# Kernel optimization log

Hardware: AMD Instinct MI355X
Metric: run time of the kernel (lower is better)

The kernel has to match this reference:

```python
import jax, jax.numpy as jnp
import numpy as np
import math

D_K = 8  # = n_wires; one input value encoded per wire


def setup_inputs() -> dict:
    key = jax.random.key(0)
    k1, k2, k3, k4 = jax.random.split(key, 4)
    B, S, E = 4, 2048, 1024
    x = jax.random.normal(k1, (B, S, E), dtype=jnp.float32)
    theta = jax.random.normal(k2, (D_K,), dtype=jnp.float32)  # shared RX params (one ModuleList reused per head)
    W = jax.random.normal(k3, (E, E), dtype=jnp.float32) * (1.0 / math.sqrt(E))
    b = jax.random.normal(k4, (E,), dtype=jnp.float32) * 0.01
    return {"x": x, "theta": theta, "W": W, "b": b}


def reference(x, theta, W, b):
    B, S, E = x.shape
    dk = theta.shape[0]
    H = E // dk
    # Quantum circuit collapse: RX(x_i) then RX(theta_i) on |0>, measure PauliZ
    # on each wire of a product state -> <Z_i> = cos(x_i + theta_i).
    proj = x.reshape(B, S, H, dk)
    q_out = jnp.cos(proj + theta)  # theta broadcast over (B,S,H)
    # NOTE: faithful to original — attention is over the HEAD axis: (B,S,H,H)
    attn = jnp.einsum('bshd,bsgd->bshg', q_out, q_out) / math.sqrt(dk)
    attn = jax.nn.softmax(attn, axis=-1)  # dropout is identity at inference
    out = jnp.einsum('bshg,bsgd->bshd', attn, q_out)  # (B,S,H,dk)
    # faithful transpose(1,2).contiguous().view(B,S,E) reinterleave
    out = jnp.transpose(out, (0, 2, 1, 3)).reshape(B, S, E)
    return out @ W.T + b
```

## Files before the change

kernel.cpp:

```cpp
#include <hip/hip_runtime.h>
#include <hip/hip_bf16.h>
#include <stdint.h>

typedef __attribute__((ext_vector_type(8))) short bf16x8;
typedef __attribute__((ext_vector_type(4))) float f32x4;
typedef __attribute__((ext_vector_type(16))) float f32x16;
typedef __attribute__((ext_vector_type(2))) unsigned int uint32x2;
typedef __attribute__((address_space(3))) void lds_t;
typedef __attribute__((address_space(1))) void glb_t;

#define B_ 4
#define S_ 2048
#define E_ 1024
#define M_ (B_*S_)
#define QTS 152
#define PPB 2

static __device__ __forceinline__ ushort f2bf(float f) {
  uint32_t u = __float_as_uint(f);
  u += 0x7fffu + ((u >> 16) & 1u);
  return (ushort)(u >> 16);
}

static __device__ __forceinline__ uint32_t pk_bf16(float lo, float hi) {
  uint32_t r;
  asm("v_cvt_pk_bf16_f32 %0, %1, %2" : "=v"(r) : "v"(lo), "v"(hi));
  return r;
}
static __device__ __forceinline__ float fexp2(float x) {
  float r;
  asm("v_exp_f32 %0, %1" : "=v"(r) : "v"(x));
  return r;
}

static __device__ __forceinline__ void half_zip(uint32_t a, uint32_t b, bool convA,
                                                uint32_t& X, uint32_t& Y) {
  if (convA) {
    uint32x2 r = __builtin_amdgcn_permlane32_swap(b, a, false, false);
    Y = r[0]; X = r[1];
  } else {
    uint32x2 r = __builtin_amdgcn_permlane32_swap(a, b, false, false);
    X = r[0]; Y = r[1];
  }
}

__global__ __launch_bounds__(256) void qattn(const float* __restrict__ x,
                                             const float* __restrict__ theta,
                                             ushort* __restrict__ outr) {
  const int wave = threadIdx.x >> 6;
  const int lane = threadIdx.x & 63;
  const int l31 = lane & 31, hw = lane >> 5;

  const int bid = blockIdx.x;
  const int pair = (bid & 7) * 512 + (bid >> 3);

  __shared__ __align__(16) ushort qL[PPB][129 * 8];
  __shared__ __align__(16) ushort qT[PPB][16 * QTS];

  uint32x2 pr = __builtin_amdgcn_permlane32_swap((uint32_t)lane, (uint32_t)(lane + 1000),
                                                 false, false);
  const bool convA = (__builtin_amdgcn_readfirstlane((int)pr[0]) >= 1000);

  auto gen = [&](int bs_g, int sel) {
    ushort* qpg = qL[sel];
    ushort* qtg = qT[sel];
    const int h  = 32 * wave + (lane >> 1);
    const int dh = (lane & 1) * 4;
    const float4 xv = *(const float4*)(x + (size_t)bs_g * E_ + h * 8 + dh);
    float q[4];
    q[0] = __cosf(xv.x + theta[dh + 0]);
    q[1] = __cosf(xv.y + theta[dh + 1]);
    q[2] = __cosf(xv.z + theta[dh + 2]);
    q[3] = __cosf(xv.w + theta[dh + 3]);

    const float QS = 0.71419165f;
    uint2 pw;
    pw.x = pk_bf16(q[0] * QS, q[1] * QS);
    pw.y = pk_bf16(q[2] * QS, q[3] * QS);
    *(uint2*)(qpg + h * 8 + dh) = pw;

    #pragma unroll
    for (int j = 0; j < 4; ++j)
      qtg[(dh + j) * QTS + h] = f2bf(q[j]);
    #pragma unroll
    for (int j = 0; j < 4; ++j)
      qtg[(8 + dh + j) * QTS + h] = (j == 0) ? (ushort)0x3F80u : (ushort)0u;

    if (lane == 0) *(uint4*)(qpg + 128 * 8) = make_uint4(0, 0, 0, 0);
  };

  gen(pair * PPB + 0, 0);
  gen(pair * PPB + 1, 1);
  __syncthreads();
  __builtin_amdgcn_sched_barrier(0);

  const int hi = wave;
  const bf16x8 zf = {};

  #pragma unroll
  for (int pp = 0; pp < PPB; ++pp) {
    const ushort* qp = qL[pp];
    const ushort* qt = qT[pp];
    const int bs = pair * PPB + pp;
    const int b = bs >> 11, s = bs & 2047;

    bf16x8 aqv[4];
    #pragma unroll
    for (int gj = 0; gj < 4; ++gj) {
      const int arow = (lane < 32) ? (gj * 32 + l31) : 128;
      aqv[gj] = *(const bf16x8*)(qp + arow * 8);
    }
    const int brow = (lane < 32) ? (hi * 32 + l31) : 128;
    const bf16x8 bq = *(const bf16x8*)(qp + brow * 8);

    f32x16 oacc = {};

    #pragma unroll
    for (int gj = 0; gj < 4; ++gj) {
      f32x16 sc = {};
      sc = __builtin_amdgcn_mfma_f32_32x32x16_bf16(aqv[gj], bq, sc, 0, 0, 0);
      bf16x8 fA = *(const bf16x8*)(qt + (l31 & 15) * QTS + (gj * 2 + 0) * 16 + hw * 8);
      bf16x8 fB = *(const bf16x8*)(qt + (l31 & 15) * QTS + (gj * 2 + 1) * 16 + hw * 8);
      fA = (l31 < 16) ? fA : zf;
      fB = (l31 < 16) ? fB : zf;
      float pv[16];
      #pragma unroll
      for (int k = 0; k < 16; ++k) pv[k] = fexp2(sc[k]);
      #pragma unroll
      for (int sl = 0; sl < 2; ++sl) {
        const int pb = sl * 8;
        const uint32_t u = pk_bf16(pv[pb+0], pv[pb+1]);
        const uint32_t v = pk_bf16(pv[pb+2], pv[pb+3]);
        const uint32_t w = pk_bf16(pv[pb+4], pv[pb+5]);
        const uint32_t z = pk_bf16(pv[pb+6], pv[pb+7]);
        uint32_t f0, f1, f2, f3;
        half_zip(u, w, convA, f0, f2);
        half_zip(v, z, convA, f1, f3);
        uint32_t fr[4] = {f0, f1, f2, f3};
        oacc = __builtin_amdgcn_mfma_f32_32x32x16_bf16((sl == 0) ? fA : fB,
                                                       *(const bf16x8*)fr,
                                                       oacc, 0, 0, 0);
      }
    }

    const int scol = s & 127, srow = s >> 7;
    const float inv = __builtin_amdgcn_rcpf(oacc[4]);
    const uint32_t o01 = pk_bf16(oacc[0] * inv, oacc[1] * inv);
    const uint32_t o23 = pk_bf16(oacc[2] * inv, oacc[3] * inv);
    const int h = hi * 32 + l31;
    const size_t row = (size_t)(b * 2048 + h * 16 + srow);
    *(uint2*)(outr + row * E_ + scol * 8 + hw * 4) = make_uint2(o01, o23);
  }
}

__global__ __launch_bounds__(256) void wconv(const float* __restrict__ W,
                                             ushort* __restrict__ Wb) {
  const int i = blockIdx.x * 256 + threadIdx.x;
  const float4 v = ((const float4*)W)[i];
  ushort4 o;
  o.x = f2bf(v.x); o.y = f2bf(v.y); o.z = f2bf(v.z); o.w = f2bf(v.w);
  ((ushort4*)Wb)[i] = o;
}

__global__ __launch_bounds__(256) void gemm_bt(const ushort* __restrict__ A,
                                               const ushort* __restrict__ Bw,
                                               const float* __restrict__ bias,
                                               float* __restrict__ C) {
  __shared__ __align__(16) ushort As[128 * 32];
  __shared__ __align__(16) ushort Bs[128 * 32];

  const int t = threadIdx.x;
  const int lane = t & 63;
  const int wavei = t >> 6;
  const int wr = wavei >> 1, wc = wavei & 1;
  const int lhi = lane >> 4, llo = lane & 15;
  const size_t ar0 = (size_t)blockIdx.x * 128;
  const size_t br0 = (size_t)blockIdx.y * 128;

  const int c0 = t, c1 = t + 256;
  const int r0 = c0 >> 2, kp0 = (c0 & 3) * 8;
  const int r1 = c1 >> 2, kp1 = (c1 & 3) * 8;

  f32x4 acc[4][4] = {};

  for (int k0 = 0; k0 < E_; k0 += 32) {
    __builtin_amdgcn_global_load_lds((const glb_t*)(A  + (ar0 + r0) * E_ + k0 + kp0),
                                     (lds_t*)(As + c0 * 8), 16, 0, 0);
    __builtin_amdgcn_global_load_lds((const glb_t*)(A  + (ar0 + r1) * E_ + k0 + kp1),
                                     (lds_t*)(As + c1 * 8), 16, 0, 0);
    __builtin_amdgcn_global_load_lds((const glb_t*)(Bw + (br0 + r0) * E_ + k0 + kp0),
                                     (lds_t*)(Bs + c0 * 8), 16, 0, 0);
    __builtin_amdgcn_global_load_lds((const glb_t*)(Bw + (br0 + r1) * E_ + k0 + kp1),
                                     (lds_t*)(Bs + c1 * 8), 16, 0, 0);
    __syncthreads();

    bf16x8 af[4], bfr[4];
    #pragma unroll
    for (int i = 0; i < 4; ++i)
      af[i] = *(const bf16x8*)(As + (wr * 64 + i * 16 + llo) * 32 + lhi * 8);
    #pragma unroll
    for (int j = 0; j < 4; ++j)
      bfr[j] = *(const bf16x8*)(Bs + (wc * 64 + j * 16 + llo) * 32 + lhi * 8);

    #pragma unroll
    for (int i = 0; i < 4; ++i)
      #pragma unroll
      for (int j = 0; j < 4; ++j)
        acc[i][j] = __builtin_amdgcn_mfma_f32_16x16x32_bf16(af[i], bfr[j], acc[i][j], 0, 0, 0);

    __syncthreads();
  }

  #pragma unroll
  for (int j = 0; j < 4; ++j) {
    const int n = (int)br0 + wc * 64 + j * 16 + llo;
    const float bj = bias[n];
    #pragma unroll
    for (int i = 0; i < 4; ++i) {
      const int mb = (int)ar0 + wr * 64 + i * 16 + lhi * 4;
      #pragma unroll
      for (int r = 0; r < 4; ++r) {
        C[(size_t)(mb + r) * E_ + n] = acc[i][j][r] + bj;
      }
    }
  }
}

extern "C" void kernel_launch(void* const* d_in, const int* in_sizes, int n_in,
                              void* d_out, int out_size, void* d_ws, size_t ws_size,
                              hipStream_t stream) {
  const float* x     = (const float*)d_in[0];
  const float* theta = (const float*)d_in[1];
  const float* W     = (const float*)d_in[2];
  const float* bias  = (const float*)d_in[3];
  float* out = (float*)d_out;

  ushort* outr = (ushort*)d_ws;
  ushort* Wb   = (ushort*)((char*)d_ws + (size_t)M_ * E_ * 2);

  qattn<<<M_ / PPB, 256, 0, stream>>>(x, theta, outr);
  wconv<<<(E_ * E_) / (256 * 4), 256, 0, stream>>>(W, Wb);
  dim3 g(M_ / 128, E_ / 128);
  gemm_bt<<<g, 256, 0, stream>>>(outr, Wb, bias, out);
}
```

Baseline: 70.46 us.

## Double-buffer GEMM LDS tiles and trim attention kernel padding writes

The GEMM now uses two LDS buffers. The next K-slice's global-to-LDS loads are issued before computing on the current slice, so memory latency can overlap with the MFMA work. In the attention kernel, the zero-fill writes for unused padding rows and the per-lane zero select are dropped, because those output rows are never read. The PV accumulation is also split across two independent accumulators to shorten the MFMA dependency chain. This relies on the end-of-loop barrier also waiting for the async loads to land, and it doubles the GEMM's LDS use.

```diff
diff --git a/kernel.cpp b/kernel.cpp
--- a/kernel.cpp
+++ b/kernel.cpp
@@ -82,9 +82,7 @@
     #pragma unroll
     for (int j = 0; j < 4; ++j)
       qtg[(dh + j) * QTS + h] = f2bf(q[j]);
-    #pragma unroll
-    for (int j = 0; j < 4; ++j)
-      qtg[(8 + dh + j) * QTS + h] = (j == 0) ? (ushort)0x3F80u : (ushort)0u;
+    qtg[(8 + dh) * QTS + h] = (ushort)0x3F80u;
 
     if (lane == 0) *(uint4*)(qpg + 128 * 8) = make_uint4(0, 0, 0, 0);
   };
@@ -95,7 +93,6 @@
   __builtin_amdgcn_sched_barrier(0);
 
   const int hi = wave;
-  const bf16x8 zf = {};
 
   #pragma unroll
   for (int pp = 0; pp < PPB; ++pp) {
@@ -112,17 +109,16 @@
     }
     const int brow = (lane < 32) ? (hi * 32 + l31) : 128;
     const bf16x8 bq = *(const bf16x8*)(qp + brow * 8);
-
-    f32x16 oacc = {};
+    const ushort* qtb = qt + (l31 & 15) * QTS + hw * 8;
+
+    f32x16 oaccA = {}, oaccB = {};
 
     #pragma unroll
     for (int gj = 0; gj < 4; ++gj) {
       f32x16 sc = {};
       sc = __builtin_amdgcn_mfma_f32_32x32x16_bf16(aqv[gj], bq, sc, 0, 0, 0);
-      bf16x8 fA = *(const bf16x8*)(qt + (l31 & 15) * QTS + (gj * 2 + 0) * 16 + hw * 8);
-      bf16x8 fB = *(const bf16x8*)(qt + (l31 & 15) * QTS + (gj * 2 + 1) * 16 + hw * 8);
-      fA = (l31 < 16) ? fA : zf;
-      fB = (l31 < 16) ? fB : zf;
+      const bf16x8 fA = *(const bf16x8*)(qtb + (gj * 2 + 0) * 16);
+      const bf16x8 fB = *(const bf16x8*)(qtb + (gj * 2 + 1) * 16);
       float pv[16];
       #pragma unroll
       for (int k = 0; k < 16; ++k) pv[k] = fexp2(sc[k]);
@@ -137,11 +133,15 @@
         half_zip(u, w, convA, f0, f2);
         half_zip(v, z, convA, f1, f3);
         uint32_t fr[4] = {f0, f1, f2, f3};
-        oacc = __builtin_amdgcn_mfma_f32_32x32x16_bf16((sl == 0) ? fA : fB,
-                                                       *(const bf16x8*)fr,
-                                                       oacc, 0, 0, 0);
+        if (gj < 2)
+          oaccA = __builtin_amdgcn_mfma_f32_32x32x16_bf16((sl == 0) ? fA : fB,
+                                                          *(const bf16x8*)fr, oaccA, 0, 0, 0);
+        else
+          oaccB = __builtin_amdgcn_mfma_f32_32x32x16_bf16((sl == 0) ? fA : fB,
+                                                          *(const bf16x8*)fr, oaccB, 0, 0, 0);
       }
     }
+    const f32x16 oacc = oaccA + oaccB;
 
     const int scol = s & 127, srow = s >> 7;
     const float inv = __builtin_amdgcn_rcpf(oacc[4]);
@@ -166,8 +166,8 @@
                                                const ushort* __restrict__ Bw,
                                                const float* __restrict__ bias,
                                                float* __restrict__ C) {
-  __shared__ __align__(16) ushort As[128 * 32];
-  __shared__ __align__(16) ushort Bs[128 * 32];
+  __shared__ __align__(16) ushort As[2][128 * 32];
+  __shared__ __align__(16) ushort Bs[2][128 * 32];
 
   const int t = threadIdx.x;
   const int lane = t & 63;
@@ -181,26 +181,33 @@
   const int r0 = c0 >> 2, kp0 = (c0 & 3) * 8;
   const int r1 = c1 >> 2, kp1 = (c1 & 3) * 8;
 
+  auto stage = [&](int buf, int k0) {
+    __builtin_amdgcn_global_load_lds((const glb_t*)(A  + (ar0 + r0) * E_ + k0 + kp0),
+                                     (lds_t*)(As[buf] + c0 * 8), 16, 0, 0);
+    __builtin_amdgcn_global_load_lds((const glb_t*)(A  + (ar0 + r1) * E_ + k0 + kp1),
+                                     (lds_t*)(As[buf] + c1 * 8), 16, 0, 0);
+    __builtin_amdgcn_global_load_lds((const glb_t*)(Bw + (br0 + r0) * E_ + k0 + kp0),
+                                     (lds_t*)(Bs[buf] + c0 * 8), 16, 0, 0);
+    __builtin_amdgcn_global_load_lds((const glb_t*)(Bw + (br0 + r1) * E_ + k0 + kp1),
+                                     (lds_t*)(Bs[buf] + c1 * 8), 16, 0, 0);
+  };
+
   f32x4 acc[4][4] = {};
 
+  stage(0, 0);
+  __syncthreads();
+
   for (int k0 = 0; k0 < E_; k0 += 32) {
-    __builtin_amdgcn_global_load_lds((const glb_t*)(A  + (ar0 + r0) * E_ + k0 + kp0),
-                                     (lds_t*)(As + c0 * 8), 16, 0, 0);
-    __builtin_amdgcn_global_load_lds((const glb_t*)(A  + (ar0 + r1) * E_ + k0 + kp1),
-                                     (lds_t*)(As + c1 * 8), 16, 0, 0);
-    __builtin_amdgcn_global_load_lds((const glb_t*)(Bw + (br0 + r0) * E_ + k0 + kp0),
-                                     (lds_t*)(Bs + c0 * 8), 16, 0, 0);
-    __builtin_amdgcn_global_load_lds((const glb_t*)(Bw + (br0 + r1) * E_ + k0 + kp1),
-                                     (lds_t*)(Bs + c1 * 8), 16, 0, 0);
-    __syncthreads();
+    const int cur = (k0 >> 5) & 1;
+    if (k0 + 32 < E_) stage(cur ^ 1, k0 + 32);
 
     bf16x8 af[4], bfr[4];
     #pragma unroll
     for (int i = 0; i < 4; ++i)
-      af[i] = *(const bf16x8*)(As + (wr * 64 + i * 16 + llo) * 32 + lhi * 8);
+      af[i] = *(const bf16x8*)(As[cur] + (wr * 64 + i * 16 + llo) * 32 + lhi * 8);
     #pragma unroll
     for (int j = 0; j < 4; ++j)
-      bfr[j] = *(const bf16x8*)(Bs + (wc * 64 + j * 16 + llo) * 32 + lhi * 8);
+      bfr[j] = *(const bf16x8*)(Bs[cur] + (wc * 64 + j * 16 + llo) * 32 + lhi * 8);
 
     #pragma unroll
     for (int i = 0; i < 4; ++i)
```

After: 69.67 us. About the same (-1.1%).
